# Performance work log

Hardware: AMD Instinct MI355X
Metric: run time of the kernel (lower is better)

## Reference

```python
import jax, jax.numpy as jnp
import numpy as np


def setup_inputs() -> dict:
    key = jax.random.key(0)
    ks = jax.random.split(key, 6)
    B, T, C, H, E = 4, 2048, 768, 3072, 16
    scale = 0.02
    return {
        "x": jax.random.normal(ks[0], (B, T, C), dtype=jnp.float32),
        "w_shared_fc": jax.random.normal(ks[1], (C, 2 * H), dtype=jnp.float32) * scale,
        "w_shared_proj": jax.random.normal(ks[2], (H, C), dtype=jnp.float32) * scale,
        "w_experts_fc": jax.random.normal(ks[3], (E, C, 2 * H), dtype=jnp.float32) * scale,
        "w_experts_proj": jax.random.normal(ks[4], (E, H, C), dtype=jnp.float32) * scale,
        "w_gate": jax.random.normal(ks[5], (C, E), dtype=jnp.float32) * scale,
        "expert_bias": jnp.zeros((E,), dtype=jnp.float32),
        "top_k": 4,
    }


def _swiglu(h):
    gate, val = jnp.split(h, 2, axis=-1)
    return jax.nn.silu(gate) * val


def reference(x, w_shared_fc, w_shared_proj, w_experts_fc, w_experts_proj,
              w_gate, expert_bias, top_k):
    B, T, C = x.shape
    E = expert_bias.shape[0]
    N = B * T

    # shared expert (applied to every token)
    shared = _swiglu(x @ w_shared_fc) @ w_shared_proj  # [B,T,C]

    # top-k sigmoid routing
    gate_logits = x @ w_gate + expert_bias            # [B,T,E]
    gate_w = jax.nn.sigmoid(gate_logits)
    top_w, top_idx = jax.lax.top_k(gate_w, top_k)     # [B,T,K]
    top_w = top_w / jnp.sum(top_w, axis=-1, keepdims=True)

    # dense per-token/per-expert weight matrix [N,E] (zero for unrouted)
    w_dense = jnp.sum(jax.nn.one_hot(top_idx, E, dtype=x.dtype) * top_w[..., None],
                      axis=-2).reshape(N, E)

    flat_x = x.reshape(N, C)

    def body(acc, params):
        wfc, wproj, we = params  # [C,2H], [H,C], [N]
        out = _swiglu(flat_x @ wfc) @ wproj  # [N,C]
        return acc + we[:, None] * out, None

    routed, _ = jax.lax.scan(body, jnp.zeros_like(flat_x),
                             (w_experts_fc, w_experts_proj, w_dense.T))
    return shared + routed.reshape(B, T, C)
```

## Files before the change

### kernel.cpp

```cpp
#include <hip/hip_runtime.h>
#include <hip/hip_bf16.h>

typedef __hip_bfloat16 bf16;
typedef __attribute__((ext_vector_type(8))) short short8;
typedef __attribute__((ext_vector_type(4))) float float4v;

#define BK 32

__device__ __forceinline__ void gload16(const bf16* g, bf16* s) {
    __builtin_amdgcn_global_load_lds(
        (const __attribute__((address_space(1))) void*)g,
        (__attribute__((address_space(3))) void*)s, 16, 0, 0);
}


__global__ void k_zero_cnt(int* cnt) {
    if (threadIdx.x < 16) cnt[threadIdx.x] = 0;
}

__global__ void k_convert_x(const float* __restrict__ in, bf16* __restrict__ out, int n) {
    int i = (blockIdx.x * blockDim.x + threadIdx.x) * 4;
    if (i + 3 < n) {
        float4 v = *(const float4*)(in + i);
        out[i + 0] = __float2bfloat16(v.x);
        out[i + 1] = __float2bfloat16(v.y);
        out[i + 2] = __float2bfloat16(v.z);
        out[i + 3] = __float2bfloat16(v.w);
    }
}

__global__ void k_transpose(const float* __restrict__ in, bf16* __restrict__ out,
                            int R, int S) {
    __shared__ float tile[32][33];
    size_t mat = (size_t)blockIdx.z * R * S;
    int s0 = blockIdx.x * 32, r0 = blockIdx.y * 32;
    int tx = threadIdx.x, ty = threadIdx.y;
    #pragma unroll
    for (int i = 0; i < 32; i += 8)
        tile[ty + i][tx] = in[mat + (size_t)(r0 + ty + i) * S + s0 + tx];
    __syncthreads();
    #pragma unroll
    for (int i = 0; i < 32; i += 8)
        out[mat + (size_t)(s0 + ty + i) * R + r0 + tx] = __float2bfloat16(tile[tx][ty + i]);
}

__global__ void k_gate(const float* __restrict__ x, const float* __restrict__ wg,
                       const float* __restrict__ bias, int* __restrict__ cnt,
                       int* __restrict__ tok, float* __restrict__ wl) {
    __shared__ float gates[16][17];
    int t = threadIdx.x;
    int tl = t >> 4;
    int e = t & 15;
    int token = blockIdx.x * 16 + tl;
    const float* xr = x + (size_t)token * 768;
    float acc = 0.f;
    #pragma unroll 4
    for (int c = 0; c < 768; ++c) acc += xr[c] * wg[c * 16 + e];
    acc += bias[e];
    gates[tl][e] = 1.f / (1.f + expf(-acc));
    __syncthreads();
    if (t < 16) {
        int token2 = blockIdx.x * 16 + t;
        float g[16];
        #pragma unroll
        for (int j = 0; j < 16; ++j) g[j] = gates[t][j];
        int idx[4]; float w[4]; float sum = 0.f;
        #pragma unroll
        for (int k = 0; k < 4; ++k) {
            float best = -1e30f; int bi = 0;
            #pragma unroll
            for (int j = 0; j < 16; ++j)
                if (g[j] > best) { best = g[j]; bi = j; }
            idx[k] = bi; w[k] = best; sum += best; g[bi] = -1e30f;
        }
        float inv = 1.f / sum;
        for (int k = 0; k < 4; ++k) {
            int slot = atomicAdd(&cnt[idx[k]], 1);
            tok[(idx[k] << 13) + slot] = token2;
            wl[(idx[k] << 13) + slot] = w[k] * inv;
        }
    }
}

__global__ void k_offsets(const int* __restrict__ cnt, int* __restrict__ offs) {
    if (threadIdx.x == 0) {
        int s = 0;
        for (int e = 0; e < 16; ++e) { offs[e] = s; s += cnt[e]; }
    }
}

template<int GATHER>
__global__ __launch_bounds__(512) void k_fc_swiglu(
    const bf16* __restrict__ A, const bf16* __restrict__ BT,
    bf16* __restrict__ act, const int* __restrict__ cnt,
    const int* __restrict__ offs, const int* __restrict__ tok) {
    const int Kd = 768, H = 3072;
    int e = blockIdx.z;
    int m0 = blockIdx.y * 128;
    int n0 = blockIdx.x * 128;
    int M;
    size_t actbase = 0;
    const int* tl = nullptr;
    if (GATHER) {
        M = cnt[e];
        if (m0 >= M) return;
        tl = tok + (e << 13);
        actbase = (size_t)offs[e] * H;
        BT += (size_t)e * 6144 * Kd;
    } else {
        M = 8192;
    }

    __shared__ bf16 sA[128 * BK];
    __shared__ bf16 sBg[128 * BK];
    __shared__ bf16 sBv[128 * BK];

    int tid = threadIdx.x;
    int lane = tid & 63;
    int w = tid >> 6;
    int wm = w & 1, wn = w >> 1;

    int sr = tid >> 2;
    int k2 = (tid & 3) ^ ((sr >> 1) & 3);

    int grA = GATHER ? tl[min(m0 + sr, M - 1)] : (m0 + sr);
    const bf16* gA  = A  + (size_t)grA * Kd + k2 * 8;
    const bf16* gBg = BT + (size_t)(n0 + sr) * Kd + k2 * 8;
    const bf16* gBv = BT + (size_t)(H + n0 + sr) * Kd + k2 * 8;
    bf16* sAp  = sA  + tid * 8;
    bf16* sBgp = sBg + tid * 8;
    bf16* sBvp = sBv + tid * 8;

    float4v ag[4][2] = {};
    float4v av[4][2] = {};
    int quad = lane >> 4, l16 = lane & 15;
    int q2 = quad ^ ((l16 >> 1) & 3);

    for (int k0 = 0; k0 < Kd; k0 += BK) {
        __syncthreads();
        gload16(gA + k0, sAp);
        gload16(gBg + k0, sBgp);
        gload16(gBv + k0, sBvp);
        __syncthreads();
        short8 af[4], bg[2], bv[2];
        #pragma unroll
        for (int mf = 0; mf < 4; ++mf) {
            int row = wm * 64 + mf * 16 + l16;
            af[mf] = *(const short8*)(sA + row * BK + q2 * 8);
        }
        #pragma unroll
        for (int nf = 0; nf < 2; ++nf) {
            int row = wn * 32 + nf * 16 + l16;
            bg[nf] = *(const short8*)(sBg + row * BK + q2 * 8);
            bv[nf] = *(const short8*)(sBv + row * BK + q2 * 8);
        }
        #pragma unroll
        for (int mf = 0; mf < 4; ++mf)
            #pragma unroll
            for (int nf = 0; nf < 2; ++nf) {
                ag[mf][nf] = __builtin_amdgcn_mfma_f32_16x16x32_bf16(af[mf], bg[nf], ag[mf][nf], 0, 0, 0);
                av[mf][nf] = __builtin_amdgcn_mfma_f32_16x16x32_bf16(af[mf], bv[nf], av[mf][nf], 0, 0, 0);
            }
    }

    #pragma unroll
    for (int mf = 0; mf < 4; ++mf)
        #pragma unroll
        for (int nf = 0; nf < 2; ++nf)
            #pragma unroll
            for (int r = 0; r < 4; ++r) {
                int mrow = m0 + wm * 64 + mf * 16 + quad * 4 + r;
                if (GATHER && mrow >= M) continue;
                int col = n0 + wn * 32 + nf * 16 + l16;
                float g = ag[mf][nf][r];
                float v = av[mf][nf][r];
                float sg = g / (1.f + __expf(-g));
                act[actbase + (size_t)mrow * H + col] = __float2bfloat16(sg * v);
            }
}

template<int ROUTED>
__global__ __launch_bounds__(512) void k_proj(
    const bf16* __restrict__ Aact, const bf16* __restrict__ PT,
    float* __restrict__ out, const int* __restrict__ cnt,
    const int* __restrict__ offs, const int* __restrict__ tok,
    const float* __restrict__ wl) {
    const int Kd = 3072;
    int e = blockIdx.z;
    int m0 = blockIdx.y * 256;
    int n0 = blockIdx.x * 128;
    int M;
    size_t abase = 0;
    if (ROUTED) {
        M = cnt[e];
        if (m0 >= M) return;
        abase = (size_t)offs[e] * Kd;
        PT += (size_t)e * 768 * Kd;
    } else {
        M = 8192;
    }

    __shared__ bf16 sA[256 * BK];
    __shared__ bf16 sB[128 * BK];

    int tid = threadIdx.x, lane = tid & 63, w = tid >> 6;
    int wm = w & 3, wn = w >> 2;

    int srA0 = tid >> 2;
    int srA1 = (tid + 512) >> 2;
    int k2A0 = (tid & 3) ^ ((srA0 >> 1) & 3);
    int k2A1 = (tid & 3) ^ ((srA1 >> 1) & 3);
    int srB = tid >> 2;
    int k2B = (tid & 3) ^ ((srB >> 1) & 3);

    int ra0 = min(m0 + srA0, M - 1);
    int ra1 = min(m0 + srA1, M - 1);
    const bf16* gA0 = Aact + abase + (size_t)ra0 * Kd + k2A0 * 8;
    const bf16* gA1 = Aact + abase + (size_t)ra1 * Kd + k2A1 * 8;
    const bf16* gB  = PT + (size_t)(n0 + srB) * Kd + k2B * 8;
    bf16* sA0p = sA + tid * 8;
    bf16* sA1p = sA + (tid + 512) * 8;
    bf16* sBp  = sB + tid * 8;

    float4v acc[4][4] = {};
    int quad = lane >> 4, l16 = lane & 15;
    int q2 = quad ^ ((l16 >> 1) & 3);

    for (int kk = 0; kk < Kd; kk += BK) {
        __syncthreads();
        gload16(gA0 + kk, sA0p);
        gload16(gA1 + kk, sA1p);
        gload16(gB + kk, sBp);
        __syncthreads();
        short8 af[4], bb[4];
        #pragma unroll
        for (int i = 0; i < 4; ++i) {
            int rowa = wm * 64 + i * 16 + l16;
            int rowb = wn * 64 + i * 16 + l16;
            af[i] = *(const short8*)(sA + rowa * BK + q2 * 8);
            bb[i] = *(const short8*)(sB + rowb * BK + q2 * 8);
        }
        #pragma unroll
        for (int mf = 0; mf < 4; ++mf)
            #pragma unroll
            for (int nf = 0; nf < 4; ++nf)
                acc[mf][nf] = __builtin_amdgcn_mfma_f32_16x16x32_bf16(af[mf], bb[nf], acc[mf][nf], 0, 0, 0);
    }

    #pragma unroll
    for (int mf = 0; mf < 4; ++mf) {
        #pragma unroll
        for (int r = 0; r < 4; ++r) {
            int mr = m0 + wm * 64 + mf * 16 + quad * 4 + r;
            if (ROUTED) {
                if (mr < M) {
                    int t = tok[(e << 13) + mr];
                    float wgt = wl[(e << 13) + mr];
                    #pragma unroll
                    for (int nf = 0; nf < 4; ++nf) {
                        int col = n0 + wn * 64 + nf * 16 + l16;
                        atomicAdd(out + (size_t)t * 768 + col, wgt * acc[mf][nf][r]);
                    }
                }
            } else {
                #pragma unroll
                for (int nf = 0; nf < 4; ++nf) {
                    int col = n0 + wn * 64 + nf * 16 + l16;
                    out[(size_t)mr * 768 + col] = acc[mf][nf][r];
                }
            }
        }
    }
}


extern "C" void kernel_launch(void* const* d_in, const int* in_sizes, int n_in,
                              void* d_out, int out_size, void* d_ws, size_t ws_size,
                              hipStream_t stream) {
    const float* x    = (const float*)d_in[0];
    const float* wfc  = (const float*)d_in[1];
    const float* wpr  = (const float*)d_in[2];
    const float* wefc = (const float*)d_in[3];
    const float* wepr = (const float*)d_in[4];
    const float* wg   = (const float*)d_in[5];
    const float* eb   = (const float*)d_in[6];
    float* out = (float*)d_out;

    char* p = (char*)d_ws;
    bf16* x_bf  = (bf16*)p; p += (size_t)8192 * 768 * 2;
    bf16* fcT_s = (bf16*)p; p += (size_t)6144 * 768 * 2;
    bf16* prT_s = (bf16*)p; p += (size_t)768 * 3072 * 2;
    bf16* fcT_e = (bf16*)p; p += (size_t)16 * 6144 * 768 * 2;
    bf16* prT_e = (bf16*)p; p += (size_t)16 * 768 * 3072 * 2;
    bf16* act_s = (bf16*)p; p += (size_t)8192 * 3072 * 2;
    bf16* act_r = (bf16*)p; p += (size_t)32768 * 3072 * 2;
    int* cnt    = (int*)p;  p += 64;
    int* offs   = (int*)p;  p += 64;
    int* tok    = (int*)p;  p += (size_t)16 * 8192 * 4;
    float* wl   = (float*)p; p += (size_t)16 * 8192 * 4;

    k_zero_cnt<<<dim3(1), dim3(64), 0, stream>>>(cnt);
    k_convert_x<<<dim3(6144), dim3(256), 0, stream>>>(x, x_bf, 8192 * 768);
    k_transpose<<<dim3(192, 24, 1), dim3(32, 8), 0, stream>>>(wfc, fcT_s, 768, 6144);
    k_transpose<<<dim3(24, 96, 1), dim3(32, 8), 0, stream>>>(wpr, prT_s, 3072, 768);
    k_transpose<<<dim3(192, 24, 16), dim3(32, 8), 0, stream>>>(wefc, fcT_e, 768, 6144);
    k_transpose<<<dim3(24, 96, 16), dim3(32, 8), 0, stream>>>(wepr, prT_e, 3072, 768);
    k_gate<<<dim3(512), dim3(256), 0, stream>>>(x, wg, eb, cnt, tok, wl);
    k_offsets<<<dim3(1), dim3(64), 0, stream>>>(cnt, offs);

    k_fc_swiglu<0><<<dim3(24, 64, 1), dim3(512), 0, stream>>>(x_bf, fcT_s, act_s, cnt, offs, tok);
    k_fc_swiglu<1><<<dim3(24, 64, 16), dim3(512), 0, stream>>>(x_bf, fcT_e, act_r, cnt, offs, tok);
    k_proj<0><<<dim3(6, 32, 1), dim3(512), 0, stream>>>(act_s, prT_s, out, cnt, offs, tok, wl);
    k_proj<1><<<dim3(6, 32, 16), dim3(512), 0, stream>>>(act_r, prT_e, out, cnt, offs, tok, wl);
}
```

Measured before the change: 1.649 ms.

## Replace routed atomic scatter with dense store plus per-token combine; vectorize transpose

The routed projection now writes weighted expert outputs densely into a compact buffer (reusing the expert FC weight workspace) instead of issuing float atomicAdds to scattered token rows. A new combine kernel then sums each token's four expert contributions into the output, using a per-token slot map recorded by the gating kernel. This targets atomic contention and traffic, at the cost of an extra buffer round trip. Separately, the weight transpose now uses float4 loads and 8-byte bf16 stores with a 1D block, and the counter zeroing is folded into the x conversion kernel to save a launch.

```diff
diff --git a/kernel.cpp b/kernel.cpp
--- a/kernel.cpp
+++ b/kernel.cpp
@@ -14,11 +14,9 @@
 }
 
 
-__global__ void k_zero_cnt(int* cnt) {
-    if (threadIdx.x < 16) cnt[threadIdx.x] = 0;
-}
-
-__global__ void k_convert_x(const float* __restrict__ in, bf16* __restrict__ out, int n) {
+__global__ void k_convert_x(const float* __restrict__ in, bf16* __restrict__ out,
+                            int n, int* __restrict__ cnt) {
+    if (blockIdx.x == 0 && threadIdx.x < 16) cnt[threadIdx.x] = 0;
     int i = (blockIdx.x * blockDim.x + threadIdx.x) * 4;
     if (i + 3 < n) {
         float4 v = *(const float4*)(in + i);
@@ -34,19 +32,23 @@
     __shared__ float tile[32][33];
     size_t mat = (size_t)blockIdx.z * R * S;
     int s0 = blockIdx.x * 32, r0 = blockIdx.y * 32;
-    int tx = threadIdx.x, ty = threadIdx.y;
+    int tid = threadIdx.x;
+    int rr = tid >> 3, sc = (tid & 7) * 4;
+    float4 v = *(const float4*)(in + mat + (size_t)(r0 + rr) * S + s0 + sc);
+    tile[rr][sc + 0] = v.x; tile[rr][sc + 1] = v.y;
+    tile[rr][sc + 2] = v.z; tile[rr][sc + 3] = v.w;
+    __syncthreads();
+    int ss = tid >> 3, rc = (tid & 7) * 4;
+    bf16 tmp[4];
     #pragma unroll
-    for (int i = 0; i < 32; i += 8)
-        tile[ty + i][tx] = in[mat + (size_t)(r0 + ty + i) * S + s0 + tx];
-    __syncthreads();
-    #pragma unroll
-    for (int i = 0; i < 32; i += 8)
-        out[mat + (size_t)(s0 + ty + i) * R + r0 + tx] = __float2bfloat16(tile[tx][ty + i]);
+    for (int i = 0; i < 4; ++i) tmp[i] = __float2bfloat16(tile[rc + i][ss]);
+    *(uint2*)(out + mat + (size_t)(s0 + ss) * R + r0 + rc) = *(uint2*)tmp;
 }
 
 __global__ void k_gate(const float* __restrict__ x, const float* __restrict__ wg,
                        const float* __restrict__ bias, int* __restrict__ cnt,
-                       int* __restrict__ tok, float* __restrict__ wl) {
+                       int* __restrict__ tok, float* __restrict__ wl,
+                       int* __restrict__ slotk) {
     __shared__ float gates[16][17];
     int t = threadIdx.x;
     int tl = t >> 4;
@@ -78,6 +80,7 @@
             int slot = atomicAdd(&cnt[idx[k]], 1);
             tok[(idx[k] << 13) + slot] = token2;
             wl[(idx[k] << 13) + slot] = w[k] * inv;
+            slotk[token2 * 4 + k] = (idx[k] << 13) | slot;
         }
     }
 }
@@ -87,6 +90,24 @@
         int s = 0;
         for (int e = 0; e < 16; ++e) { offs[e] = s; s += cnt[e]; }
     }
+}
+
+__global__ __launch_bounds__(192) void k_combine(
+    const float* __restrict__ routed, const int* __restrict__ slotk,
+    const int* __restrict__ offs, float* __restrict__ out) {
+    int t = blockIdx.x;
+    int c4 = threadIdx.x * 4;
+    float* op = out + (size_t)t * 768 + c4;
+    float4 acc = *(float4*)op;
+    #pragma unroll
+    for (int k = 0; k < 4; ++k) {
+        int sk = slotk[t * 4 + k];
+        int e = sk >> 13, sl = sk & 8191;
+        const float* row = routed + (size_t)(offs[e] + sl) * 768 + c4;
+        float4 v = *(const float4*)row;
+        acc.x += v.x; acc.y += v.y; acc.z += v.z; acc.w += v.w;
+    }
+    *(float4*)op = acc;
 }
 
 template<int GATHER>
@@ -183,18 +204,19 @@
 __global__ __launch_bounds__(512) void k_proj(
     const bf16* __restrict__ Aact, const bf16* __restrict__ PT,
     float* __restrict__ out, const int* __restrict__ cnt,
-    const int* __restrict__ offs, const int* __restrict__ tok,
-    const float* __restrict__ wl) {
+    const int* __restrict__ offs, const float* __restrict__ wl) {
     const int Kd = 3072;
     int e = blockIdx.z;
     int m0 = blockIdx.y * 256;
     int n0 = blockIdx.x * 128;
     int M;
     size_t abase = 0;
+    int roffs = 0;
     if (ROUTED) {
         M = cnt[e];
         if (m0 >= M) return;
-        abase = (size_t)offs[e] * Kd;
+        roffs = offs[e];
+        abase = (size_t)roffs * Kd;
         PT += (size_t)e * 768 * Kd;
     } else {
         M = 8192;
@@ -254,12 +276,12 @@
             int mr = m0 + wm * 64 + mf * 16 + quad * 4 + r;
             if (ROUTED) {
                 if (mr < M) {
-                    int t = tok[(e << 13) + mr];
                     float wgt = wl[(e << 13) + mr];
+                    float* orow = out + (size_t)(roffs + mr) * 768;
                     #pragma unroll
                     for (int nf = 0; nf < 4; ++nf) {
                         int col = n0 + wn * 64 + nf * 16 + l16;
-                        atomicAdd(out + (size_t)t * 768 + col, wgt * acc[mf][nf][r]);
+                        orow[col] = wgt * acc[mf][nf][r];
                     }
                 }
             } else {
@@ -298,18 +320,20 @@
     int* offs   = (int*)p;  p += 64;
     int* tok    = (int*)p;  p += (size_t)16 * 8192 * 4;
     float* wl   = (float*)p; p += (size_t)16 * 8192 * 4;
-
-    k_zero_cnt<<<dim3(1), dim3(64), 0, stream>>>(cnt);
-    k_convert_x<<<dim3(6144), dim3(256), 0, stream>>>(x, x_bf, 8192 * 768);
-    k_transpose<<<dim3(192, 24, 1), dim3(32, 8), 0, stream>>>(wfc, fcT_s, 768, 6144);
-    k_transpose<<<dim3(24, 96, 1), dim3(32, 8), 0, stream>>>(wpr, prT_s, 3072, 768);
-    k_transpose<<<dim3(192, 24, 16), dim3(32, 8), 0, stream>>>(wefc, fcT_e, 768, 6144);
-    k_transpose<<<dim3(24, 96, 16), dim3(32, 8), 0, stream>>>(wepr, prT_e, 3072, 768);
-    k_gate<<<dim3(512), dim3(256), 0, stream>>>(x, wg, eb, cnt, tok, wl);
+    int* slotk  = (int*)p;  p += (size_t)8192 * 4 * 4;
+    float* routed_out = (float*)fcT_e;
+
+    k_convert_x<<<dim3(6144), dim3(256), 0, stream>>>(x, x_bf, 8192 * 768, cnt);
+    k_transpose<<<dim3(192, 24, 1), dim3(256), 0, stream>>>(wfc, fcT_s, 768, 6144);
+    k_transpose<<<dim3(24, 96, 1), dim3(256), 0, stream>>>(wpr, prT_s, 3072, 768);
+    k_transpose<<<dim3(192, 24, 16), dim3(256), 0, stream>>>(wefc, fcT_e, 768, 6144);
+    k_transpose<<<dim3(24, 96, 16), dim3(256), 0, stream>>>(wepr, prT_e, 3072, 768);
+    k_gate<<<dim3(512), dim3(256), 0, stream>>>(x, wg, eb, cnt, tok, wl, slotk);
     k_offsets<<<dim3(1), dim3(64), 0, stream>>>(cnt, offs);
 
     k_fc_swiglu<0><<<dim3(24, 64, 1), dim3(512), 0, stream>>>(x_bf, fcT_s, act_s, cnt, offs, tok);
     k_fc_swiglu<1><<<dim3(24, 64, 16), dim3(512), 0, stream>>>(x_bf, fcT_e, act_r, cnt, offs, tok);
-    k_proj<0><<<dim3(6, 32, 1), dim3(512), 0, stream>>>(act_s, prT_s, out, cnt, offs, tok, wl);
-    k_proj<1><<<dim3(6, 32, 16), dim3(512), 0, stream>>>(act_r, prT_e, out, cnt, offs, tok, wl);
-}
+    k_proj<0><<<dim3(6, 32, 1), dim3(512), 0, stream>>>(act_s, prT_s, out, cnt, offs, wl);
+    k_proj<1><<<dim3(6, 32, 16), dim3(512), 0, stream>>>(act_r, prT_e, routed_out, cnt, offs, wl);
+    k_combine<<<dim3(8192), dim3(192), 0, stream>>>(routed_out, slotk, offs, out);
+}
```

After: 1.652 ms. Within noise of the previous version (+0.2%).
